# Kernel tuning notes

Hardware: AMD Instinct MI355X
Metric: run time of the kernel (lower is better)

## Reference

```python
import jax, jax.numpy as jnp
import numpy as np
from jax import lax

N, T, V, E, H, D, B = 16384, 16, 10000, 256, 256, 512, 128


def setup_inputs() -> dict:
    key = jax.random.key(0)
    ks = jax.random.split(key, 12)
    tok = jax.random.randint(ks[0], (N, T), 1, V)
    lens = jax.random.randint(ks[1], (N,), 4, T + 1)
    tok = jnp.where(jnp.arange(T)[None, :] < lens[:, None], tok, 0)  # pad_id = 0
    ast_path_len = jnp.full((B,), N // B, dtype=jnp.int32)  # 128 paths per sample
    u = lambda k, s: jax.random.uniform(k, s, jnp.float32, -0.1, 0.1)
    emb = u(ks[2], (V, E)).at[0].set(0.0)  # padding_idx=0 row zeroed
    return {
        "ast_path": tok,
        "ast_path_len": ast_path_len,
        "emb": emb,
        "W_ih_f": u(ks[3], (4 * H, E)), "W_hh_f": u(ks[4], (4 * H, H)), "b_f": u(ks[5], (4 * H,)),
        "W_ih_b": u(ks[6], (4 * H, E)), "W_hh_b": u(ks[7], (4 * H, H)), "b_b": u(ks[8], (4 * H,)),
        "W_lin": u(ks[9], (D, 2 * H)), "b_lin": jnp.zeros((D,), jnp.float32),
    }


def _lstm_final_h(x_tm, lens, W_ih, W_hh, b, reverse):
    # x_tm: [T, N, E]; returns final hidden state [N, H] honoring per-seq length
    n = x_tm.shape[1]
    h0 = jnp.zeros((n, H), x_tm.dtype)

    def step(carry, xt):
        h, c = carry
        x, t = xt
        gates = x @ W_ih.T + h @ W_hh.T + b  # [N, 4H]
        i, f, g, o = jnp.split(gates, 4, axis=-1)
        c_new = jax.nn.sigmoid(f) * c + jax.nn.sigmoid(i) * jnp.tanh(g)
        h_new = jax.nn.sigmoid(o) * jnp.tanh(c_new)
        m = (t < lens)[:, None]  # packed-sequence semantics: frozen past length
        return (jnp.where(m, h_new, h), jnp.where(m, c_new, c)), None

    (h, _), _ = lax.scan(step, (h0, h0), (x_tm, jnp.arange(x_tm.shape[0])), reverse=reverse)
    return h


def reference(ast_path, ast_path_len, emb, W_ih_f, W_hh_f, b_f, W_ih_b, W_hh_b, b_b, W_lin, b_lin):
    lens = (ast_path != 0).sum(axis=-1)  # pad_id = 0
    x = emb[ast_path]                     # [N, T, E]; dropout is identity at eval
    x_tm = jnp.swapaxes(x, 0, 1)          # [T, N, E]
    h_fwd = _lstm_final_h(x_tm, lens, W_ih_f, W_hh_f, b_f, reverse=False)
    h_bwd = _lstm_final_h(x_tm, lens, W_ih_b, W_hh_b, b_b, reverse=True)
    h_n = jnp.concatenate([h_fwd, h_bwd], axis=1)        # [N, 2H]
    repr_ = h_n @ W_lin.T + b_lin                         # [N, D]
    # segment-mean pooling over path groups (replaces the Python loop)
    n_paths = repr_.shape[0]
    seg_ids = jnp.repeat(jnp.arange(ast_path_len.shape[0]), ast_path_len,
                         total_repeat_length=n_paths)
    sums = jax.ops.segment_sum(repr_, seg_ids, num_segments=ast_path_len.shape[0])
    pooled = sums / ast_path_len[:, None].astype(repr_.dtype)  # [B, D]
    norm = jnp.sqrt(jnp.sum(pooled * pooled, axis=-1, keepdims=True))
    return pooled / jnp.maximum(norm, 1e-5)
```

## Files before the change

### kernel.cpp

```cpp
#include <hip/hip_runtime.h>
#include <stdint.h>

#define N_SEQ 16384
#define T_LEN 16
#define E_DIM 256
#define H_DIM 256
#define K_DIM 512
#define B_SAMP 128
#define V_SIZE 10000

typedef __bf16 bf16x8 __attribute__((ext_vector_type(8)));
typedef float  f32x4  __attribute__((ext_vector_type(4)));
typedef unsigned short ush;

__device__ __forceinline__ ush f2bf(float x) {
  unsigned int u = __float_as_uint(x);
  u = (u + 0x7fffu + ((u >> 16) & 1u)) >> 16;
  return (ush)u;
}
__device__ __forceinline__ float bf2f(ush v) {
  return __uint_as_float(((unsigned int)v) << 16);
}
__device__ __forceinline__ float sigmoidf_(float x) {
  return 1.0f / (1.0f + __expf(-x));
}
__device__ __forceinline__ float tanhf_(float x) {
  float e = __expf(2.0f * x);
  return 1.0f - 2.0f / (e + 1.0f);
}
__device__ __forceinline__ void glds16(const void* g, const void* l) {
  __builtin_amdgcn_global_load_lds(
      (const __attribute__((address_space(1))) unsigned int*)g,
      (__attribute__((address_space(3))) unsigned int*)l, 16, 0, 0);
}


__global__ __launch_bounds__(256) void k_lens(const int* __restrict__ tok, int* __restrict__ lens,
                                              int* __restrict__ hist) {
  __shared__ int lh[17];
  if (threadIdx.x < 17) lh[threadIdx.x] = 0;
  __syncthreads();
  int n = blockIdx.x * 256 + threadIdx.x;
  const int* r = tok + n * T_LEN;
  int c = 0;
#pragma unroll
  for (int t = 0; t < T_LEN; ++t) c += (r[t] != 0);
  lens[n] = c;
  atomicAdd(&lh[c], 1);
  __syncthreads();
  if (threadIdx.x < 17 && lh[threadIdx.x]) atomicAdd(&hist[threadIdx.x], lh[threadIdx.x]);
}

__global__ void k_offsets(const int* __restrict__ hist, int* __restrict__ cursor,
                          int* __restrict__ cnts_f, int* __restrict__ cnts_b) {
  if (threadIdx.x == 0) {
    int off = 0;
    for (int l = 16; l >= 0; --l) { cursor[l] = off; off += hist[l]; }
    for (int t = 0; t < 16; ++t) {
      int cf = 0, cb = 0;
      for (int l = t; l <= 16; ++l) cf += hist[l];
      for (int l = t + 1; l <= 16; ++l) cb += hist[l];
      cnts_f[t] = cf;
      cnts_b[t] = cb;
    }
  }
}

__global__ __launch_bounds__(256) void k_scatter(const int* __restrict__ lens, int* __restrict__ cursor,
                                                 int* __restrict__ perm, int* __restrict__ pinv,
                                                 int* __restrict__ plens) {
  int n = blockIdx.x * 256 + threadIdx.x;
  int l = lens[n];
  int pos = atomicAdd(&cursor[l], 1);
  perm[pos] = n;
  pinv[n] = pos;
  plens[pos] = l;
}

__global__ __launch_bounds__(256) void k_tokperm(const int* __restrict__ tok, const int* __restrict__ perm,
                                                 int* __restrict__ tokperm) {
  int id = blockIdx.x * 256 + threadIdx.x;
  int t = id >> 14;
  int pos = id & (N_SEQ - 1);
  tokperm[id] = tok[perm[pos] * T_LEN + t];
}

__global__ __launch_bounds__(256) void k_embcvt(const float* __restrict__ emb, ush* __restrict__ out) {
  int i = blockIdx.x * 256 + threadIdx.x;
  out[i] = f2bf(emb[i]);
}

__global__ __launch_bounds__(256) void k_wprep(const float* __restrict__ Wih_f, const float* __restrict__ Whh_f,
                                               const float* __restrict__ Wih_b, const float* __restrict__ Whh_b,
                                               ush* __restrict__ wpt_f, ush* __restrict__ wpt_b) {
  int id = blockIdx.x * 256 + threadIdx.x;
  int dir = id >> 19;
  int rem = id & ((1 << 19) - 1);
  int p = rem >> 9;
  int k = rem & 511;
  int nb = p >> 8, wc = (p >> 6) & 3, q = (p >> 4) & 3, jj = p & 15;
  int r = q * 256 + nb * 64 + wc * 16 + jj;
  const float* Wih = dir ? Wih_b : Wih_f;
  const float* Whh = dir ? Whh_b : Whh_f;
  float v = (k < 256) ? Wih[r * 256 + k] : Whh[r * 256 + (k - 256)];
  ush* o = dir ? wpt_b : wpt_f;
  o[p * 512 + k] = f2bf(v);
}


__global__ __launch_bounds__(512, 4)
void k_step(const ush* __restrict__ embbf, const int* __restrict__ tokperm,
            const int* __restrict__ plens,
            const int* __restrict__ cnts_f, const int* __restrict__ cnts_b,
            const ush* __restrict__ wpt_f, const ush* __restrict__ wpt_b,
            const float* __restrict__ bias_f, const float* __restrict__ bias_b,
            const ush* __restrict__ hr_f, ush* __restrict__ hw_f,
            const ush* __restrict__ hr_b, ush* __restrict__ hw_b,
            float* __restrict__ cT_f, float* __restrict__ cT_b,
            int s) {
  const int b = blockIdx.x;
  const int dir = b & 1;
  const int nblk = (b & 7) >> 1;
  const int rt = b >> 3;
  const int t = dir ? (15 - s) : s;
  const int cnt = dir ? cnts_b[t] : cnts_f[t];
  const int m0 = rt * 128;
  if (m0 >= cnt) return;

  const ush* wpt = dir ? wpt_b : wpt_f;
  const float* bias = dir ? bias_b : bias_f;
  const ush* hr = dir ? hr_b : hr_f;
  ush* hw = dir ? hw_b : hw_f;
  float* cT = dir ? cT_b : cT_f;

  __shared__ __align__(128) unsigned char ldsA[128 * 128];
  __shared__ __align__(128) unsigned char ldsB[256 * 128];

  const int tid = threadIdx.x;
  const int lane = tid & 63;
  const int w = tid >> 6;
  const int wr = w >> 2;
  const int wc = w & 3;

  const int l8 = lane >> 3;
  const int l7 = lane & 7;
  const int arow0 = 16 * w + l8;
  const int arow1 = arow0 + 8;
  const int ach0 = l7 ^ (arow0 & 7);
  const int ach1 = l7 ^ (arow1 & 7);
  const unsigned aoffE0 = (unsigned)tokperm[t * N_SEQ + m0 + arow0] * E_DIM + ach0 * 8;
  const unsigned aoffE1 = (unsigned)tokperm[t * N_SEQ + m0 + arow1] * E_DIM + ach1 * 8;
  const unsigned aoffH0 = (unsigned)(m0 + arow0) * H_DIM + ach0 * 8;
  const unsigned aoffH1 = (unsigned)(m0 + arow1) * H_DIM + ach1 * 8;
  unsigned boff[4];
#pragma unroll
  for (int j = 0; j < 4; ++j) {
    const int brow = 32 * w + 8 * j + l8;
    const int bch = l7 ^ (brow & 7);
    boff[j] = (unsigned)(nblk * 256 + brow) * K_DIM + bch * 8;
  }

  f32x4 acc[4][4] = {};
  const int frow = lane & 15;
  const int fkq = lane >> 4;

  for (int kt = 0; kt < 8; ++kt) {
    const int k0 = kt * 64;
    if (kt < 4) {
      glds16(embbf + aoffE0 + k0, &ldsA[(16 * w) * 128]);
      glds16(embbf + aoffE1 + k0, &ldsA[(16 * w + 8) * 128]);
    } else {
      glds16(hr + aoffH0 + (k0 - E_DIM), &ldsA[(16 * w) * 128]);
      glds16(hr + aoffH1 + (k0 - E_DIM), &ldsA[(16 * w + 8) * 128]);
    }
#pragma unroll
    for (int j = 0; j < 4; ++j)
      glds16(wpt + boff[j] + k0, &ldsB[(32 * w + 8 * j) * 128]);
    __syncthreads();
#pragma unroll
    for (int ksub = 0; ksub < 2; ++ksub) {
      bf16x8 av[4], bv[4];
#pragma unroll
      for (int fr = 0; fr < 4; ++fr) {
        const int row = wr * 64 + fr * 16 + frow;
        const int ch = (ksub * 4 + fkq) ^ (row & 7);
        av[fr] = *(const bf16x8*)&ldsA[row * 128 + ch * 16];
      }
#pragma unroll
      for (int fc = 0; fc < 4; ++fc) {
        const int row = wc * 64 + fc * 16 + frow;
        const int ch = (ksub * 4 + fkq) ^ (row & 7);
        bv[fc] = *(const bf16x8*)&ldsB[row * 128 + ch * 16];
      }
      __builtin_amdgcn_s_setprio(1);
#pragma unroll
      for (int fr = 0; fr < 4; ++fr)
#pragma unroll
        for (int fc = 0; fc < 4; ++fc)
          acc[fr][fc] = __builtin_amdgcn_mfma_f32_16x16x32_bf16(av[fr], bv[fc], acc[fr][fc], 0, 0, 0);
      __builtin_amdgcn_s_setprio(0);
    }
    __syncthreads();
  }

  const int j = nblk * 64 + wc * 16 + frow;
  const float b0 = bias[j], b1 = bias[256 + j], b2 = bias[512 + j], b3 = bias[768 + j];
#pragma unroll
  for (int fr = 0; fr < 4; ++fr) {
    const int n0 = m0 + wr * 64 + fr * 16 + fkq * 4;
    const int4 l4 = *(const int4*)&plens[n0];
    f32x4 cv = *(const f32x4*)&cT[(size_t)j * N_SEQ + n0];
    const f32x4 gi = acc[fr][0], gf = acc[fr][1], gg = acc[fr][2], go = acc[fr][3];
#pragma unroll
    for (int r = 0; r < 4; ++r) {
      const int lnv = (r == 0) ? l4.x : (r == 1) ? l4.y : (r == 2) ? l4.z : l4.w;
      const size_t hidx = (size_t)(n0 + r) * H_DIM + j;
      if (t < lnv) {
        const float iv = sigmoidf_(gi[r] + b0);
        const float fv = sigmoidf_(gf[r] + b1);
        const float gv = tanhf_(gg[r] + b2);
        const float ov = sigmoidf_(go[r] + b3);
        const bool first = dir ? (t == lnv - 1) : (t == 0);
        const float cn = fv * (first ? 0.0f : cv[r]) + iv * gv;
        cv[r] = cn;
        hw[hidx] = f2bf(ov * tanhf_(cn));
      } else if (!dir) {
        hw[hidx] = hr[hidx];
      }
    }
    *(f32x4*)&cT[(size_t)j * N_SEQ + n0] = cv;
  }
}


__global__ __launch_bounds__(256) void k_pool(const ush* __restrict__ hf,
                                              const ush* __restrict__ hb,
                                              const int* __restrict__ pinv,
                                              const int* __restrict__ plen,
                                              float* __restrict__ pooled) {
  const int b = blockIdx.x, tid = threadIdx.x;
  int start = 0;
  for (int i = 0; i < b; ++i) start += plen[i];
  const int cnt = plen[b];
  float s0 = 0.f, s1 = 0.f;
  for (int r = 0; r < cnt; ++r) {
    const size_t pr = (size_t)pinv[start + r];
    s0 += bf2f(hf[pr * H_DIM + tid]);
    s1 += bf2f(hb[pr * H_DIM + tid]);
  }
  float inv = 1.0f / (float)cnt;
  pooled[b * 512 + tid] = s0 * inv;
  pooled[b * 512 + H_DIM + tid] = s1 * inv;
}


__global__ __launch_bounds__(256) void k_final(const float* __restrict__ pooled,
                                               const float* __restrict__ W,
                                               const float* __restrict__ bl,
                                               float* __restrict__ out) {
  const int b = blockIdx.x, tid = threadIdx.x;
  __shared__ float pv[512];
  __shared__ float pre[512];
  __shared__ float red[4];
  pv[tid] = pooled[b * 512 + tid];
  pv[tid + 256] = pooled[b * 512 + 256 + tid];
  __syncthreads();
#pragma unroll
  for (int half = 0; half < 2; ++half) {
    const int dd = tid + half * 256;
    const f32x4* wr = (const f32x4*)(W + (size_t)dd * 512);
    const f32x4* pvv = (const f32x4*)pv;
    float s = bl[dd];
#pragma unroll 4
    for (int k4 = 0; k4 < 128; ++k4) {
      f32x4 wv = wr[k4], xv = pvv[k4];
      s += wv[0] * xv[0] + wv[1] * xv[1] + wv[2] * xv[2] + wv[3] * xv[3];
    }
    pre[dd] = s;
  }
  __syncthreads();
  float ss = pre[tid] * pre[tid] + pre[tid + 256] * pre[tid + 256];
#pragma unroll
  for (int off = 32; off > 0; off >>= 1) ss += __shfl_down(ss, off, 64);
  if ((tid & 63) == 0) red[tid >> 6] = ss;
  __syncthreads();
  float tot = red[0] + red[1] + red[2] + red[3];
  float scale = 1.0f / fmaxf(sqrtf(tot), 1e-5f);
  out[b * 512 + tid] = pre[tid] * scale;
  out[b * 512 + 256 + tid] = pre[tid + 256] * scale;
}


extern "C" void kernel_launch(void* const* d_in, const int* in_sizes, int n_in,
                              void* d_out, int out_size, void* d_ws, size_t ws_size,
                              hipStream_t stream) {
  const int* tok    = (const int*)d_in[0];
  const int* plen   = (const int*)d_in[1];
  const float* emb  = (const float*)d_in[2];
  const float* Wih_f = (const float*)d_in[3];
  const float* Whh_f = (const float*)d_in[4];
  const float* b_f   = (const float*)d_in[5];
  const float* Wih_b = (const float*)d_in[6];
  const float* Whh_b = (const float*)d_in[7];
  const float* b_b   = (const float*)d_in[8];
  const float* Wlin  = (const float*)d_in[9];
  const float* blin  = (const float*)d_in[10];
  float* out = (float*)d_out;

  char* ws = (char*)d_ws;
  size_t off = 0;
  auto alloc = [&](size_t bytes) {
    void* p = ws + off;
    off = (off + bytes + 255) & ~(size_t)255;
    return p;
  };
  ush* embbf   = (ush*)alloc((size_t)V_SIZE * E_DIM * 2);
  ush* wptf    = (ush*)alloc((size_t)1024 * K_DIM * 2);
  ush* wptb    = (ush*)alloc((size_t)1024 * K_DIM * 2);
  int* lens    = (int*)alloc((size_t)N_SEQ * 4);
  int* perm    = (int*)alloc((size_t)N_SEQ * 4);
  int* pinv    = (int*)alloc((size_t)N_SEQ * 4);
  int* plens   = (int*)alloc((size_t)N_SEQ * 4);
  int* tokperm = (int*)alloc((size_t)T_LEN * N_SEQ * 4);
  int* hist    = (int*)alloc(17 * 4);
  int* cursor  = (int*)alloc(17 * 4);
  int* cntsf   = (int*)alloc(16 * 4);
  int* cntsb   = (int*)alloc(16 * 4);
  ush* h0f     = (ush*)alloc((size_t)N_SEQ * H_DIM * 2);
  ush* h1f     = (ush*)alloc((size_t)N_SEQ * H_DIM * 2);
  ush* h0b     = (ush*)alloc((size_t)N_SEQ * H_DIM * 2);
  ush* h1b     = (ush*)alloc((size_t)N_SEQ * H_DIM * 2);
  float* cTf   = (float*)alloc((size_t)H_DIM * N_SEQ * 4);
  float* cTb   = (float*)alloc((size_t)H_DIM * N_SEQ * 4);
  float* pooled = (float*)alloc((size_t)B_SAMP * 512 * 4);

  hipMemsetAsync(hist, 0, 17 * 4, stream);
  hipMemsetAsync(h0f, 0, (size_t)N_SEQ * H_DIM * 2, stream);
  hipMemsetAsync(h1f, 0, (size_t)N_SEQ * H_DIM * 2, stream);
  hipMemsetAsync(h0b, 0, (size_t)N_SEQ * H_DIM * 2, stream);
  hipMemsetAsync(h1b, 0, (size_t)N_SEQ * H_DIM * 2, stream);

  k_lens<<<N_SEQ / 256, 256, 0, stream>>>(tok, lens, hist);
  k_offsets<<<1, 64, 0, stream>>>(hist, cursor, cntsf, cntsb);
  k_scatter<<<N_SEQ / 256, 256, 0, stream>>>(lens, cursor, perm, pinv, plens);
  k_tokperm<<<(T_LEN * N_SEQ) / 256, 256, 0, stream>>>(tok, perm, tokperm);
  k_embcvt<<<(V_SIZE * E_DIM) / 256, 256, 0, stream>>>(emb, embbf);
  k_wprep<<<(2 * 1024 * K_DIM) / 256, 256, 0, stream>>>(Wih_f, Whh_f, Wih_b, Whh_b, wptf, wptb);

  for (int s = 0; s < T_LEN; ++s) {
    const ush* hrf = (s & 1) ? h1f : h0f;
    ush* hwf       = (s & 1) ? h0f : h1f;
    const ush* hrb = (s & 1) ? h1b : h0b;
    ush* hwb       = (s & 1) ? h0b : h1b;
    k_step<<<1024, 512, 0, stream>>>(embbf, tokperm, plens, cntsf, cntsb, wptf, wptb,
                                     b_f, b_b, hrf, hwf, hrb, hwb, cTf, cTb, s);
  }
  k_pool<<<B_SAMP, 256, 0, stream>>>(h0f, h0b, pinv, plen, pooled);
  k_final<<<B_SAMP, 256, 0, stream>>>(pooled, Wlin, blin, out);
}
```

Measured before the change: 936.2 us.

## Double-buffer LDS in LSTM step GEMM and shrink tile to 128x128

Reworks the per-timestep LSTM gate GEMM kernel: blocks drop from 512 to 256 threads with a 128x128 output tile (32 hidden units per gate), and the grid doubles to 2048 blocks. Weight prep is re-laid-out to match the narrower column blocks. The K loop now double-buffers A/B tiles in LDS, prefetching two stages ahead and using explicit vmcnt waits and barriers so global-to-LDS loads overlap MFMA compute. The aim is to hide load latency and improve occupancy, at the cost of more LDS per block and more redundant A-tile loads across column blocks.

```diff
diff --git a/kernel.cpp b/kernel.cpp
--- a/kernel.cpp
+++ b/kernel.cpp
@@ -98,8 +98,8 @@
   int rem = id & ((1 << 19) - 1);
   int p = rem >> 9;
   int k = rem & 511;
-  int nb = p >> 8, wc = (p >> 6) & 3, q = (p >> 4) & 3, jj = p & 15;
-  int r = q * 256 + nb * 64 + wc * 16 + jj;
+  int nb = p >> 7, wcl = (p >> 6) & 1, q = (p >> 4) & 3, jj = p & 15;
+  int r = q * 256 + nb * 32 + wcl * 16 + jj;
   const float* Wih = dir ? Wih_b : Wih_f;
   const float* Whh = dir ? Whh_b : Whh_f;
   float v = (k < 256) ? Wih[r * 256 + k] : Whh[r * 256 + (k - 256)];
@@ -108,7 +108,7 @@
 }
 
 
-__global__ __launch_bounds__(512, 4)
+__global__ __launch_bounds__(256, 2)
 void k_step(const ush* __restrict__ embbf, const int* __restrict__ tokperm,
             const int* __restrict__ plens,
             const int* __restrict__ cnts_f, const int* __restrict__ cnts_b,
@@ -120,8 +120,8 @@
             int s) {
   const int b = blockIdx.x;
   const int dir = b & 1;
-  const int nblk = (b & 7) >> 1;
-  const int rt = b >> 3;
+  const int nblk = ((b >> 1) & 3) * 2 + ((b >> 3) & 1);
+  const int rt = b >> 4;
   const int t = dir ? (15 - s) : s;
   const int cnt = dir ? cnts_b[t] : cnts_f[t];
   const int m0 = rt * 128;
@@ -133,64 +133,60 @@
   ush* hw = dir ? hw_b : hw_f;
   float* cT = dir ? cT_b : cT_f;
 
-  __shared__ __align__(128) unsigned char ldsA[128 * 128];
-  __shared__ __align__(128) unsigned char ldsB[256 * 128];
+  __shared__ __align__(128) unsigned char lds[2][32768];
 
   const int tid = threadIdx.x;
   const int lane = tid & 63;
   const int w = tid >> 6;
-  const int wr = w >> 2;
-  const int wc = w & 3;
-
-  const int l8 = lane >> 3;
-  const int l7 = lane & 7;
-  const int arow0 = 16 * w + l8;
-  const int arow1 = arow0 + 8;
-  const int ach0 = l7 ^ (arow0 & 7);
-  const int ach1 = l7 ^ (arow1 & 7);
-  const unsigned aoffE0 = (unsigned)tokperm[t * N_SEQ + m0 + arow0] * E_DIM + ach0 * 8;
-  const unsigned aoffE1 = (unsigned)tokperm[t * N_SEQ + m0 + arow1] * E_DIM + ach1 * 8;
-  const unsigned aoffH0 = (unsigned)(m0 + arow0) * H_DIM + ach0 * 8;
-  const unsigned aoffH1 = (unsigned)(m0 + arow1) * H_DIM + ach1 * 8;
-  unsigned boff[4];
-#pragma unroll
-  for (int j = 0; j < 4; ++j) {
-    const int brow = 32 * w + 8 * j + l8;
-    const int bch = l7 ^ (brow & 7);
-    boff[j] = (unsigned)(nblk * 256 + brow) * K_DIM + bch * 8;
-  }
+  const int wr = w >> 1, wc = w & 1;
+  const int l8 = lane >> 3, l7 = lane & 7;
+  const int frow = lane & 15, fkq = lane >> 4;
+
+  unsigned aoffE[4], aoffH[4], boff[4];
+#pragma unroll
+  for (int i = 0; i < 4; ++i) {
+    const int arow = 32 * w + 8 * i + l8;
+    const int ach = l7 ^ (arow & 7);
+    aoffE[i] = (unsigned)tokperm[t * N_SEQ + m0 + arow] * (E_DIM * 2) + ach * 16;
+    aoffH[i] = (unsigned)(m0 + arow) * (H_DIM * 2) + ach * 16;
+    boff[i]  = (unsigned)(nblk * 128 + arow) * (K_DIM * 2) + ach * 16;
+  }
+  const char* embc = (const char*)embbf;
+  const char* hrc  = (const char*)hr;
+  const char* wptc = (const char*)wpt;
 
   f32x4 acc[4][4] = {};
-  const int frow = lane & 15;
-  const int fkq = lane >> 4;
-
-  for (int kt = 0; kt < 8; ++kt) {
-    const int k0 = kt * 64;
+
+  auto stage = [&](int kt, int buf) {
     if (kt < 4) {
-      glds16(embbf + aoffE0 + k0, &ldsA[(16 * w) * 128]);
-      glds16(embbf + aoffE1 + k0, &ldsA[(16 * w + 8) * 128]);
+      const int ak = kt * 128;
+#pragma unroll
+      for (int i = 0; i < 4; ++i)
+        glds16(embc + aoffE[i] + ak, &lds[buf][(32 * w + 8 * i) * 128]);
     } else {
-      glds16(hr + aoffH0 + (k0 - E_DIM), &ldsA[(16 * w) * 128]);
-      glds16(hr + aoffH1 + (k0 - E_DIM), &ldsA[(16 * w + 8) * 128]);
-    }
-#pragma unroll
-    for (int j = 0; j < 4; ++j)
-      glds16(wpt + boff[j] + k0, &ldsB[(32 * w + 8 * j) * 128]);
-    __syncthreads();
+      const int ak = (kt - 4) * 128;
+#pragma unroll
+      for (int i = 0; i < 4; ++i)
+        glds16(hrc + aoffH[i] + ak, &lds[buf][(32 * w + 8 * i) * 128]);
+    }
+#pragma unroll
+    for (int i = 0; i < 4; ++i)
+      glds16(wptc + boff[i] + kt * 128, &lds[buf][16384 + (32 * w + 8 * i) * 128]);
+  };
+  auto compute = [&](int buf) {
 #pragma unroll
     for (int ksub = 0; ksub < 2; ++ksub) {
+      const int slot = ksub * 4 + fkq;
       bf16x8 av[4], bv[4];
 #pragma unroll
       for (int fr = 0; fr < 4; ++fr) {
         const int row = wr * 64 + fr * 16 + frow;
-        const int ch = (ksub * 4 + fkq) ^ (row & 7);
-        av[fr] = *(const bf16x8*)&ldsA[row * 128 + ch * 16];
+        av[fr] = *(const bf16x8*)&lds[buf][row * 128 + ((slot ^ (row & 7)) * 16)];
       }
 #pragma unroll
       for (int fc = 0; fc < 4; ++fc) {
-        const int row = wc * 64 + fc * 16 + frow;
-        const int ch = (ksub * 4 + fkq) ^ (row & 7);
-        bv[fc] = *(const bf16x8*)&ldsB[row * 128 + ch * 16];
+        const int prow = wc * 64 + fc * 16 + frow;
+        bv[fc] = *(const bf16x8*)&lds[buf][16384 + prow * 128 + ((slot ^ (prow & 7)) * 16)];
       }
       __builtin_amdgcn_s_setprio(1);
 #pragma unroll
@@ -200,10 +196,25 @@
           acc[fr][fc] = __builtin_amdgcn_mfma_f32_16x16x32_bf16(av[fr], bv[fc], acc[fr][fc], 0, 0, 0);
       __builtin_amdgcn_s_setprio(0);
     }
-    __syncthreads();
-  }
-
-  const int j = nblk * 64 + wc * 16 + frow;
+  };
+
+  stage(0, 0);
+  stage(1, 1);
+#pragma unroll
+  for (int kt = 0; kt < 8; ++kt) {
+    if (kt <= 6) asm volatile("s_waitcnt vmcnt(8)" ::: "memory");
+    else         asm volatile("s_waitcnt vmcnt(0)" ::: "memory");
+    __builtin_amdgcn_s_barrier();
+    __builtin_amdgcn_sched_barrier(0);
+    compute(kt & 1);
+    if (kt <= 5) {
+      __builtin_amdgcn_s_barrier();
+      __builtin_amdgcn_sched_barrier(0);
+      stage(kt + 2, kt & 1);
+    }
+  }
+
+  const int j = nblk * 32 + wc * 16 + frow;
   const float b0 = bias[j], b1 = bias[256 + j], b2 = bias[512 + j], b3 = bias[768 + j];
 #pragma unroll
   for (int fr = 0; fr < 4; ++fr) {
@@ -352,7 +363,7 @@
     ush* hwf       = (s & 1) ? h0f : h1f;
     const ush* hrb = (s & 1) ? h1b : h0b;
     ush* hwb       = (s & 1) ? h0b : h1b;
-    k_step<<<1024, 512, 0, stream>>>(embbf, tokperm, plens, cntsf, cntsb, wptf, wptb,
+    k_step<<<2048, 256, 0, stream>>>(embbf, tokperm, plens, cntsf, cntsb, wptf, wptb,
                                      b_f, b_b, hrf, hwf, hrb, hwb, cTf, cTb, s);
   }
   k_pool<<<B_SAMP, 256, 0, stream>>>(h0f, h0b, pinv, plen, pooled);
```

New measurement: 979.5 us. 4.6% more time.

## Store LSTM cell state in bf16, skip dead writes, prefetch epilogue inputs

Applied to the files above, without the earlier changes.

The per-step cell state buffer moves from fp32 to bf16, which halves its read and write traffic every timestep. Stores of a cell-state group are skipped when every sequence in the group has passed its length. Bias, lengths and the old cell state are now loaded before the GEMM loop so their latency overlaps the MFMA work. The grid becomes 2D, with direction on y and the block's N tile mapped contiguously on x. Rounding the cell state to bf16 at each step adds accumulated error to the recurrence.

```diff
diff --git a/kernel.cpp b/kernel.cpp
--- a/kernel.cpp
+++ b/kernel.cpp
@@ -116,22 +116,21 @@
             const float* __restrict__ bias_f, const float* __restrict__ bias_b,
             const ush* __restrict__ hr_f, ush* __restrict__ hw_f,
             const ush* __restrict__ hr_b, ush* __restrict__ hw_b,
-            float* __restrict__ cT_f, float* __restrict__ cT_b,
+            ush* __restrict__ cT_f, ush* __restrict__ cT_b,
             int s) {
-  const int b = blockIdx.x;
-  const int dir = b & 1;
-  const int nblk = (b & 7) >> 1;
-  const int rt = b >> 3;
+  const int dir = blockIdx.y;
   const int t = dir ? (15 - s) : s;
   const int cnt = dir ? cnts_b[t] : cnts_f[t];
-  const int m0 = rt * 128;
+  const int mblk = blockIdx.x >> 2;
+  const int m0 = mblk * 128;
   if (m0 >= cnt) return;
 
+  const int nblk = blockIdx.x & 3;
   const ush* wpt = dir ? wpt_b : wpt_f;
   const float* bias = dir ? bias_b : bias_f;
   const ush* hr = dir ? hr_b : hr_f;
   ush* hw = dir ? hw_b : hw_f;
-  float* cT = dir ? cT_b : cT_f;
+  ush* cT = dir ? cT_b : cT_f;
 
   __shared__ __align__(128) unsigned char ldsA[128 * 128];
   __shared__ __align__(128) unsigned char ldsB[256 * 128];
@@ -141,6 +140,19 @@
   const int w = tid >> 6;
   const int wr = w >> 2;
   const int wc = w & 3;
+  const int frow = lane & 15;
+  const int fkq = lane >> 4;
+
+  const int j = nblk * 64 + wc * 16 + frow;
+  const float b0 = bias[j], b1 = bias[256 + j], b2 = bias[512 + j], b3 = bias[768 + j];
+  int4 l4[4];
+  ushort4 cvu[4];
+#pragma unroll
+  for (int fr = 0; fr < 4; ++fr) {
+    const int n0 = m0 + wr * 64 + fr * 16 + fkq * 4;
+    l4[fr] = *(const int4*)&plens[n0];
+    cvu[fr] = *(const ushort4*)&cT[(size_t)j * N_SEQ + n0];
+  }
 
   const int l8 = lane >> 3;
   const int l7 = lane & 7;
@@ -154,15 +166,13 @@
   const unsigned aoffH1 = (unsigned)(m0 + arow1) * H_DIM + ach1 * 8;
   unsigned boff[4];
 #pragma unroll
-  for (int j = 0; j < 4; ++j) {
-    const int brow = 32 * w + 8 * j + l8;
+  for (int jj = 0; jj < 4; ++jj) {
+    const int brow = 32 * w + 8 * jj + l8;
     const int bch = l7 ^ (brow & 7);
-    boff[j] = (unsigned)(nblk * 256 + brow) * K_DIM + bch * 8;
+    boff[jj] = (unsigned)(nblk * 256 + brow) * K_DIM + bch * 8;
   }
 
   f32x4 acc[4][4] = {};
-  const int frow = lane & 15;
-  const int fkq = lane >> 4;
 
   for (int kt = 0; kt < 8; ++kt) {
     const int k0 = kt * 64;
@@ -174,8 +184,8 @@
       glds16(hr + aoffH1 + (k0 - E_DIM), &ldsA[(16 * w + 8) * 128]);
     }
 #pragma unroll
-    for (int j = 0; j < 4; ++j)
-      glds16(wpt + boff[j] + k0, &ldsB[(32 * w + 8 * j) * 128]);
+    for (int jj = 0; jj < 4; ++jj)
+      glds16(wpt + boff[jj] + k0, &ldsB[(32 * w + 8 * jj) * 128]);
     __syncthreads();
 #pragma unroll
     for (int ksub = 0; ksub < 2; ++ksub) {
@@ -203,17 +213,16 @@
     __syncthreads();
   }
 
-  const int j = nblk * 64 + wc * 16 + frow;
-  const float b0 = bias[j], b1 = bias[256 + j], b2 = bias[512 + j], b3 = bias[768 + j];
 #pragma unroll
   for (int fr = 0; fr < 4; ++fr) {
     const int n0 = m0 + wr * 64 + fr * 16 + fkq * 4;
-    const int4 l4 = *(const int4*)&plens[n0];
-    f32x4 cv = *(const f32x4*)&cT[(size_t)j * N_SEQ + n0];
+    const int4 ln = l4[fr];
+    const int lmax = max(max(ln.x, ln.y), max(ln.z, ln.w));
+    float cv[4] = {bf2f(cvu[fr].x), bf2f(cvu[fr].y), bf2f(cvu[fr].z), bf2f(cvu[fr].w)};
     const f32x4 gi = acc[fr][0], gf = acc[fr][1], gg = acc[fr][2], go = acc[fr][3];
 #pragma unroll
     for (int r = 0; r < 4; ++r) {
-      const int lnv = (r == 0) ? l4.x : (r == 1) ? l4.y : (r == 2) ? l4.z : l4.w;
+      const int lnv = (r == 0) ? ln.x : (r == 1) ? ln.y : (r == 2) ? ln.z : ln.w;
       const size_t hidx = (size_t)(n0 + r) * H_DIM + j;
       if (t < lnv) {
         const float iv = sigmoidf_(gi[r] + b0);
@@ -228,7 +237,10 @@
         hw[hidx] = hr[hidx];
       }
     }
-    *(f32x4*)&cT[(size_t)j * N_SEQ + n0] = cv;
+    if (t < lmax) {
+      ushort4 cu = make_ushort4(f2bf(cv[0]), f2bf(cv[1]), f2bf(cv[2]), f2bf(cv[3]));
+      *(ushort4*)&cT[(size_t)j * N_SEQ + n0] = cu;
+    }
   }
 }
 
@@ -330,8 +342,8 @@
   ush* h1f     = (ush*)alloc((size_t)N_SEQ * H_DIM * 2);
   ush* h0b     = (ush*)alloc((size_t)N_SEQ * H_DIM * 2);
   ush* h1b     = (ush*)alloc((size_t)N_SEQ * H_DIM * 2);
-  float* cTf   = (float*)alloc((size_t)H_DIM * N_SEQ * 4);
-  float* cTb   = (float*)alloc((size_t)H_DIM * N_SEQ * 4);
+  ush* cTf     = (ush*)alloc((size_t)H_DIM * N_SEQ * 2);
+  ush* cTb     = (ush*)alloc((size_t)H_DIM * N_SEQ * 2);
   float* pooled = (float*)alloc((size_t)B_SAMP * 512 * 4);
 
   hipMemsetAsync(hist, 0, 17 * 4, stream);
@@ -347,12 +359,13 @@
   k_embcvt<<<(V_SIZE * E_DIM) / 256, 256, 0, stream>>>(emb, embbf);
   k_wprep<<<(2 * 1024 * K_DIM) / 256, 256, 0, stream>>>(Wih_f, Whh_f, Wih_b, Whh_b, wptf, wptb);
 
+  dim3 grid(512, 2);
   for (int s = 0; s < T_LEN; ++s) {
     const ush* hrf = (s & 1) ? h1f : h0f;
     ush* hwf       = (s & 1) ? h0f : h1f;
     const ush* hrb = (s & 1) ? h1b : h0b;
     ush* hwb       = (s & 1) ? h0b : h1b;
-    k_step<<<1024, 512, 0, stream>>>(embbf, tokperm, plens, cntsf, cntsb, wptf, wptb,
+    k_step<<<grid, 512, 0, stream>>>(embbf, tokperm, plens, cntsf, cntsb, wptf, wptb,
                                      b_f, b_b, hrf, hwf, hrb, hwb, cTf, cTb, s);
   }
   k_pool<<<B_SAMP, 256, 0, stream>>>(h0f, h0b, pinv, plen, pooled);
```

Result: slower. 990.4 us (+5.8%).
